# Kernel optimization log

Hardware: AMD Instinct MI355X
Metric: run time of the kernel (lower is better)

## Reference

```python
import jax, jax.numpy as jnp
import numpy as np

B, T, D, U = 64, 512, 256, 512


def setup_inputs() -> dict:
    key = jax.random.key(0)
    ks = jax.random.split(key, 7)
    s = 0.05  # keras 'uniform' init is small; small scale keeps gates unsaturated
    return {
        "x": jax.random.normal(ks[0], (B, T, D), dtype=jnp.float32),
        "w_xi": jax.random.normal(ks[1], (D, U), dtype=jnp.float32) * s,
        "w_xf": jax.random.normal(ks[2], (D, U), dtype=jnp.float32) * s,
        "w_xc": jax.random.normal(ks[3], (D, U), dtype=jnp.float32) * s,
        "w_hi": jax.random.normal(ks[4], (U, U), dtype=jnp.float32) * s,
        "w_hf": jax.random.normal(ks[5], (U, U), dtype=jnp.float32) * s,
        "w_hc": jax.random.normal(ks[6], (U, U), dtype=jnp.float32) * s,
        "b_i": jnp.zeros((1, U), dtype=jnp.float32),
        "b_f": jnp.zeros((1, U), dtype=jnp.float32),
        "b_c": jnp.zeros((1, U), dtype=jnp.float32),
        "h0": jnp.zeros((B, U), dtype=jnp.float32),
        "c0": jnp.zeros((B, U), dtype=jnp.float32),
    }


def reference(x, w_xi, w_xf, w_xc, w_hi, w_hf, w_hc, b_i, b_f, b_c, h0, c0):
    # Precompute input projections for all timesteps (batched GEMM), time-major.
    xi = (jnp.einsum('btd,du->btu', x, w_xi) + b_i).transpose(1, 0, 2)  # [T,B,U]
    xf = (jnp.einsum('btd,du->btu', x, w_xf) + b_f).transpose(1, 0, 2)
    xc = (jnp.einsum('btd,du->btu', x, w_xc) + b_c).transpose(1, 0, 2)

    def step(carry, xs):
        h, c = carry
        xi_t, xf_t, xc_t = xs
        i = jax.nn.sigmoid(xi_t + h @ w_hi)
        f = jax.nn.sigmoid(xf_t + h @ w_hf)
        c_in = jnp.tanh(xc_t + h @ w_hc)
        c_n = f * c + i * c_in
        h_n = jnp.tanh(c_n)  # output gate o == 1.0 in NOGLSTM
        return (h_n, c_n), h_n

    (_, _), hs = jax.lax.scan(step, (h0, c0), (xi, xf, xc))
    return hs.transpose(1, 0, 2)  # [B,T,U] full hidden sequence
```

## Files before the change

kernel.cpp:

```cpp
#include <hip/hip_runtime.h>
#include <stdint.h>

#define Bv 64
#define Tv 512
#define Dv 256
#define Uv 512
#define WPG 32

typedef __attribute__((ext_vector_type(8))) __bf16 bf16x8;
typedef __attribute__((ext_vector_type(8))) short short8;
typedef __attribute__((ext_vector_type(4))) float f32x4;

__device__ unsigned int g_flag[4 * WPG];
__device__ unsigned int g_gen[4 * WPG];
__device__ unsigned int g_hbuf[2 * Bv * Uv];

__device__ __forceinline__ unsigned int f2bf_bits(float x) {
    unsigned int u = __float_as_uint(x);
    return (u + 0x7fffu + ((u >> 16) & 1u)) >> 16;
}
__device__ __forceinline__ float bfbits2f(unsigned int b) {
    return __uint_as_float(b << 16);
}
__device__ __forceinline__ float fast_sigmoid(float x) {
    return __builtin_amdgcn_rcpf(1.f + __expf(-x));
}
__device__ __forceinline__ float fast_tanh(float x) {
    float ax = fabsf(x);
    float t  = __expf(-2.f * ax);
    float r  = (1.f - t) * __builtin_amdgcn_rcpf(1.f + t);
    return x < 0.f ? -r : r;
}

extern "C" __global__ void __launch_bounds__(256, 1)
noglstm_kernel(const float* __restrict__ x,
               const float* __restrict__ w_xi, const float* __restrict__ w_xf, const float* __restrict__ w_xc,
               const float* __restrict__ w_hi, const float* __restrict__ w_hf, const float* __restrict__ w_hc,
               const float* __restrict__ b_i, const float* __restrict__ b_f, const float* __restrict__ b_c,
               const float* __restrict__ h0, const float* __restrict__ c0,
               float* __restrict__ out)
{
    __shared__ f32x4 partLds[12 * 64];
    __shared__ float cTile[256];
    __shared__ float biasLds[48];
    __shared__ unsigned int baseLds;

    const int tid  = threadIdx.x;
    const int wg   = blockIdx.x;
    const int g    = wg >> 5;
    const int c    = wg & 31;
    const int r0   = g * 16;
    const int u0   = c * 16;
    const int wv   = tid >> 6;
    const int lane = tid & 63;
    const int n    = lane & 15;
    const int quad = lane >> 4;
    const int kh   = wv;
    const int m    = n;
    const int q    = quad;

    if (tid == 0) { unsigned v = g_gen[wg] + 1u; g_gen[wg] = v; baseLds = (v - 1u) * (unsigned)Tv; }
    if (tid < 16)      biasLds[tid]      = b_i[u0 + tid];
    else if (tid < 32) biasLds[tid]      = b_f[u0 + tid - 16];
    else if (tid < 48) biasLds[tid]      = b_c[u0 + tid - 32];
    cTile[tid] = c0[(size_t)(r0 + (tid >> 4)) * Uv + u0 + (tid & 15)];

    const float* WhP[3] = {w_hi, w_hf, w_hc};
    const float* WxP[3] = {w_xi, w_xf, w_xc};
    const int ucol = u0 + n;

    bf16x8 whHiR[3][4], whLoR[3][4], wxHiR[3][2], wxLoR[3][2];
    #pragma unroll
    for (int nt = 0; nt < 3; ++nt) {
        #pragma unroll
        for (int i = 0; i < 4; ++i) {
            short8 hi8, lo8;
            #pragma unroll
            for (int e = 0; e < 8; ++e) {
                int k = (kh * 4 + i) * 32 + quad * 8 + e;
                float w = WhP[nt][(size_t)k * Uv + ucol];
                unsigned int hb = f2bf_bits(w);
                unsigned int lb = f2bf_bits(w - bfbits2f(hb));
                hi8[e] = (short)hb; lo8[e] = (short)lb;
            }
            whHiR[nt][i] = __builtin_bit_cast(bf16x8, hi8);
            whLoR[nt][i] = __builtin_bit_cast(bf16x8, lo8);
        }
        #pragma unroll
        for (int i = 0; i < 2; ++i) {
            short8 hi8, lo8;
            #pragma unroll
            for (int e = 0; e < 8; ++e) {
                int k = (kh * 2 + i) * 32 + quad * 8 + e;
                float w = WxP[nt][(size_t)k * Uv + ucol];
                unsigned int hb = f2bf_bits(w);
                unsigned int lb = f2bf_bits(w - bfbits2f(hb));
                hi8[e] = (short)hb; lo8[e] = (short)lb;
            }
            wxHiR[nt][i] = __builtin_bit_cast(bf16x8, hi8);
            wxLoR[nt][i] = __builtin_bit_cast(bf16x8, lo8);
        }
    }

    bf16x8 xaH[2], xaL[2];
    #pragma unroll
    for (int i = 0; i < 2; ++i) {
        int kt = kh * 2 + i;
        const float* p = x + ((size_t)(r0 + m) * Tv + 0) * Dv + kt * 32 + q * 8;
        f32x4 a = *(const f32x4*)p;
        f32x4 b = *(const f32x4*)(p + 4);
        short8 hi8, lo8;
        #pragma unroll
        for (int e = 0; e < 8; ++e) {
            float v = (e < 4) ? a[e] : b[e - 4];
            unsigned int hb = f2bf_bits(v);
            unsigned int lb = f2bf_bits(v - bfbits2f(hb));
            hi8[e] = (short)hb; lo8[e] = (short)lb;
        }
        xaH[i] = __builtin_bit_cast(bf16x8, hi8);
        xaL[i] = __builtin_bit_cast(bf16x8, lo8);
    }
    __syncthreads();
    const unsigned int base = baseLds;

    const unsigned int* fpw = g_flag + g * WPG + kh * 8;

    for (int t = 0; t < Tv; ++t) {
        const bool packed = (t != 0);
        const bool pfch = (t + 1 < Tv);
        unsigned int hw32[32];
        f32x4 hf[8];
        f32x4 xf[4];

        if (packed) {
            const unsigned int E = base + (unsigned)t;
            unsigned int fv = 0xFFFFFFFFu;
            unsigned int spins = 0;
            for (;;) {
                if (lane < 8)
                    fv = __hip_atomic_load(fpw + lane, __ATOMIC_RELAXED,
                                           __HIP_MEMORY_SCOPE_AGENT);
                if (__all((lane >= 8) || (fv >= E))) break;
                if (++spins > (1u << 20)) break;
                if (spins > 16) __builtin_amdgcn_s_sleep(1);
            }
            __asm__ volatile("" ::: "memory");

            const unsigned int* hb = g_hbuf + (size_t)((t - 1) & 1) * (Bv * Uv);
            #pragma unroll
            for (int i = 0; i < 4; ++i) {
                int kt = kh * 4 + i;
                const unsigned int* p = hb + (size_t)(kt * 32 + q * 8) * Bv + r0 + m;
                #pragma unroll
                for (int e = 0; e < 8; ++e)
                    hw32[i * 8 + e] = __hip_atomic_load(p + e * Bv, __ATOMIC_RELAXED,
                                                        __HIP_MEMORY_SCOPE_AGENT);
            }
        } else {
            #pragma unroll
            for (int i = 0; i < 4; ++i) {
                int kt = kh * 4 + i;
                const float* p = h0 + (size_t)(r0 + m) * Uv + kt * 32 + q * 8;
                hf[i * 2]     = *(const f32x4*)p;
                hf[i * 2 + 1] = *(const f32x4*)(p + 4);
            }
        }

        if (pfch) {
            #pragma unroll
            for (int i = 0; i < 2; ++i) {
                int kt = kh * 2 + i;
                const float* p = x + ((size_t)(r0 + m) * Tv + (t + 1)) * Dv + kt * 32 + q * 8;
                xf[i * 2]     = *(const f32x4*)p;
                xf[i * 2 + 1] = *(const f32x4*)(p + 4);
            }
        }

        f32x4 acc[3], accX[3];
        #pragma unroll
        for (int nt = 0; nt < 3; ++nt) { acc[nt] = f32x4{0.f,0.f,0.f,0.f}; accX[nt] = f32x4{0.f,0.f,0.f,0.f}; }
        #pragma unroll
        for (int i = 0; i < 2; ++i) {
            #pragma unroll
            for (int nt = 0; nt < 3; ++nt) {
                accX[nt] = __builtin_amdgcn_mfma_f32_16x16x32_bf16(xaH[i], wxHiR[nt][i], accX[nt], 0, 0, 0);
                accX[nt] = __builtin_amdgcn_mfma_f32_16x16x32_bf16(xaH[i], wxLoR[nt][i], accX[nt], 0, 0, 0);
                accX[nt] = __builtin_amdgcn_mfma_f32_16x16x32_bf16(xaL[i], wxHiR[nt][i], accX[nt], 0, 0, 0);
                accX[nt] = __builtin_amdgcn_mfma_f32_16x16x32_bf16(xaL[i], wxLoR[nt][i], accX[nt], 0, 0, 0);
            }
        }

        #pragma unroll
        for (int i = 0; i < 4; ++i) {
            bf16x8 haH, haL;
            if (packed) {
                short8 hi8, lo8;
                #pragma unroll
                for (int e = 0; e < 8; ++e) {
                    unsigned int d = hw32[i * 8 + e];
                    hi8[e] = (short)(d >> 16);
                    lo8[e] = (short)(d & 0xffffu);
                }
                haH = __builtin_bit_cast(bf16x8, hi8);
                haL = __builtin_bit_cast(bf16x8, lo8);
            } else {
                short8 hi8, lo8;
                #pragma unroll
                for (int e = 0; e < 8; ++e) {
                    float v = (e < 4) ? hf[i * 2][e] : hf[i * 2 + 1][e - 4];
                    unsigned int hb2 = f2bf_bits(v);
                    unsigned int lb2 = f2bf_bits(v - bfbits2f(hb2));
                    hi8[e] = (short)hb2; lo8[e] = (short)lb2;
                }
                haH = __builtin_bit_cast(bf16x8, hi8);
                haL = __builtin_bit_cast(bf16x8, lo8);
            }
            #pragma unroll
            for (int nt = 0; nt < 3; ++nt) {
                acc[nt] = __builtin_amdgcn_mfma_f32_16x16x32_bf16(haH, whHiR[nt][i], acc[nt], 0, 0, 0);
                acc[nt] = __builtin_amdgcn_mfma_f32_16x16x32_bf16(haH, whLoR[nt][i], acc[nt], 0, 0, 0);
                acc[nt] = __builtin_amdgcn_mfma_f32_16x16x32_bf16(haL, whHiR[nt][i], acc[nt], 0, 0, 0);
                acc[nt] = __builtin_amdgcn_mfma_f32_16x16x32_bf16(haL, whLoR[nt][i], acc[nt], 0, 0, 0);
            }
        }

        #pragma unroll
        for (int nt = 0; nt < 3; ++nt) {
            acc[nt][0] += accX[nt][0]; acc[nt][1] += accX[nt][1];
            acc[nt][2] += accX[nt][2]; acc[nt][3] += accX[nt][3];
            partLds[(wv * 3 + nt) * 64 + lane] = acc[nt];
        }
        __syncthreads();

        const int r = tid >> 4, uu = tid & 15;
        float hn;
        {
            int plane = (r >> 2) * 16 + uu;
            int reg = r & 3;
            const float* pf2 = (const float*)partLds;
            float pi = biasLds[uu], pF = biasLds[16 + uu], pc = biasLds[32 + uu];
            #pragma unroll
            for (int w = 0; w < 4; ++w) {
                pi += pf2[((w * 3 + 0) * 64 + plane) * 4 + reg];
                pF += pf2[((w * 3 + 1) * 64 + plane) * 4 + reg];
                pc += pf2[((w * 3 + 2) * 64 + plane) * 4 + reg];
            }
            float iv  = fast_sigmoid(pi);
            float fv  = fast_sigmoid(pF);
            float cin = fast_tanh(pc);
            float cn  = fv * cTile[tid] + iv * cin;
            cTile[tid] = cn;
            hn = fast_tanh(cn);
            unsigned int hbb = f2bf_bits(hn);
            unsigned int lbb = f2bf_bits(hn - bfbits2f(hbb));
            __hip_atomic_store(g_hbuf + (size_t)(t & 1) * (Bv * Uv)
                               + (size_t)(u0 + uu) * Bv + (r0 + r),
                               (hbb << 16) | lbb, __ATOMIC_RELAXED,
                               __HIP_MEMORY_SCOPE_AGENT);
        }

        __asm__ volatile("s_waitcnt vmcnt(0)" ::: "memory");
        __syncthreads();
        if (tid == 0)
            __hip_atomic_store(&g_flag[g * WPG + c], base + (unsigned)t + 1u,
                               __ATOMIC_RELAXED, __HIP_MEMORY_SCOPE_AGENT);

        out[((size_t)(r0 + r) * Tv + t) * Uv + u0 + uu] = hn;

        if (pfch) {
            #pragma unroll
            for (int i = 0; i < 2; ++i) {
                short8 hi8, lo8;
                #pragma unroll
                for (int e = 0; e < 8; ++e) {
                    float v = (e < 4) ? xf[i * 2][e] : xf[i * 2 + 1][e - 4];
                    unsigned int hb2 = f2bf_bits(v);
                    unsigned int lb2 = f2bf_bits(v - bfbits2f(hb2));
                    hi8[e] = (short)hb2; lo8[e] = (short)lb2;
                }
                xaH[i] = __builtin_bit_cast(bf16x8, hi8);
                xaL[i] = __builtin_bit_cast(bf16x8, lo8);
            }
        }
        __syncthreads();
    }
}

extern "C" void kernel_launch(void* const* d_in, const int* in_sizes, int n_in,
                              void* d_out, int out_size, void* d_ws, size_t ws_size,
                              hipStream_t stream) {
    (void)in_sizes; (void)n_in; (void)out_size; (void)d_ws; (void)ws_size;
    noglstm_kernel<<<dim3(128), dim3(256), 0, stream>>>(
        (const float*)d_in[0],
        (const float*)d_in[1], (const float*)d_in[2], (const float*)d_in[3],
        (const float*)d_in[4], (const float*)d_in[5], (const float*)d_in[6],
        (const float*)d_in[7], (const float*)d_in[8], (const float*)d_in[9],
        (const float*)d_in[10], (const float*)d_in[11],
        (float*)d_out);
}
```

Measured before the change: 2.325 ms.

## Pack hidden-state exchange into 64-bit loads and move x prefetch off the critical path

Changes the global hidden-state buffer layout so adjacent unit pairs sit together, which lets each lane read h with 16 64-bit atomic loads in place of 32 32-bit loads. The next timestep's x is now issued as raw fp32 loads at the end of the step, and the bf16 hi/lo split is done at the start of the next step, overlapping the load latency with the flag spin. The trailing __syncthreads at the end of each timestep is removed, which saves one barrier per step but relies on the remaining barriers to protect shared-memory reuse across iterations.

```diff
diff --git a/kernel.cpp b/kernel.cpp
--- a/kernel.cpp
+++ b/kernel.cpp
@@ -10,10 +10,11 @@
 typedef __attribute__((ext_vector_type(8))) __bf16 bf16x8;
 typedef __attribute__((ext_vector_type(8))) short short8;
 typedef __attribute__((ext_vector_type(4))) float f32x4;
+typedef unsigned long long u64;
 
 __device__ unsigned int g_flag[4 * WPG];
 __device__ unsigned int g_gen[4 * WPG];
-__device__ unsigned int g_hbuf[2 * Bv * Uv];
+__device__ u64 g_hbuf[2 * Bv * Uv / 2];
 
 __device__ __forceinline__ unsigned int f2bf_bits(float x) {
     unsigned int u = __float_as_uint(x);
@@ -102,23 +103,13 @@
         }
     }
 
-    bf16x8 xaH[2], xaL[2];
+    f32x4 xf[4];
     #pragma unroll
     for (int i = 0; i < 2; ++i) {
         int kt = kh * 2 + i;
         const float* p = x + ((size_t)(r0 + m) * Tv + 0) * Dv + kt * 32 + q * 8;
-        f32x4 a = *(const f32x4*)p;
-        f32x4 b = *(const f32x4*)(p + 4);
-        short8 hi8, lo8;
-        #pragma unroll
-        for (int e = 0; e < 8; ++e) {
-            float v = (e < 4) ? a[e] : b[e - 4];
-            unsigned int hb = f2bf_bits(v);
-            unsigned int lb = f2bf_bits(v - bfbits2f(hb));
-            hi8[e] = (short)hb; lo8[e] = (short)lb;
-        }
-        xaH[i] = __builtin_bit_cast(bf16x8, hi8);
-        xaL[i] = __builtin_bit_cast(bf16x8, lo8);
+        xf[i * 2]     = *(const f32x4*)p;
+        xf[i * 2 + 1] = *(const f32x4*)(p + 4);
     }
     __syncthreads();
     const unsigned int base = baseLds;
@@ -128,9 +119,8 @@
     for (int t = 0; t < Tv; ++t) {
         const bool packed = (t != 0);
         const bool pfch = (t + 1 < Tv);
-        unsigned int hw32[32];
+        u64 hw64[16];
         f32x4 hf[8];
-        f32x4 xf[4];
 
         if (packed) {
             const unsigned int E = base + (unsigned)t;
@@ -146,14 +136,15 @@
             }
             __asm__ volatile("" ::: "memory");
 
-            const unsigned int* hb = g_hbuf + (size_t)((t - 1) & 1) * (Bv * Uv);
+            const u64* hb = g_hbuf + (size_t)((t - 1) & 1) * (Bv * Uv / 2);
             #pragma unroll
             for (int i = 0; i < 4; ++i) {
                 int kt = kh * 4 + i;
-                const unsigned int* p = hb + (size_t)(kt * 32 + q * 8) * Bv + r0 + m;
+                const u64* p = hb + (size_t)(kt * 16 + q * 4) * Bv + r0 + m;
                 #pragma unroll
-                for (int e = 0; e < 8; ++e)
-                    hw32[i * 8 + e] = __hip_atomic_load(p + e * Bv, __ATOMIC_RELAXED,
+                for (int j = 0; j < 4; ++j)
+                    hw64[i * 4 + j] = __hip_atomic_load(p + (size_t)j * Bv,
+                                                        __ATOMIC_RELAXED,
                                                         __HIP_MEMORY_SCOPE_AGENT);
             }
         } else {
@@ -166,14 +157,19 @@
             }
         }
 
-        if (pfch) {
-            #pragma unroll
-            for (int i = 0; i < 2; ++i) {
-                int kt = kh * 2 + i;
-                const float* p = x + ((size_t)(r0 + m) * Tv + (t + 1)) * Dv + kt * 32 + q * 8;
-                xf[i * 2]     = *(const f32x4*)p;
-                xf[i * 2 + 1] = *(const f32x4*)(p + 4);
-            }
+        bf16x8 xaH[2], xaL[2];
+        #pragma unroll
+        for (int i = 0; i < 2; ++i) {
+            short8 hi8, lo8;
+            #pragma unroll
+            for (int e = 0; e < 8; ++e) {
+                float v = (e < 4) ? xf[i * 2][e] : xf[i * 2 + 1][e - 4];
+                unsigned int hb2 = f2bf_bits(v);
+                unsigned int lb2 = f2bf_bits(v - bfbits2f(hb2));
+                hi8[e] = (short)hb2; lo8[e] = (short)lb2;
+            }
+            xaH[i] = __builtin_bit_cast(bf16x8, hi8);
+            xaL[i] = __builtin_bit_cast(bf16x8, lo8);
         }
 
         f32x4 acc[3], accX[3];
@@ -196,10 +192,14 @@
             if (packed) {
                 short8 hi8, lo8;
                 #pragma unroll
-                for (int e = 0; e < 8; ++e) {
-                    unsigned int d = hw32[i * 8 + e];
-                    hi8[e] = (short)(d >> 16);
-                    lo8[e] = (short)(d & 0xffffu);
+                for (int j = 0; j < 4; ++j) {
+                    u64 w = hw64[i * 4 + j];
+                    unsigned int d0 = (unsigned int)w;
+                    unsigned int d1 = (unsigned int)(w >> 32);
+                    hi8[2 * j]     = (short)(d0 >> 16);
+                    lo8[2 * j]     = (short)(d0 & 0xffffu);
+                    hi8[2 * j + 1] = (short)(d1 >> 16);
+                    lo8[2 * j + 1] = (short)(d1 & 0xffffu);
                 }
                 haH = __builtin_bit_cast(bf16x8, hi8);
                 haL = __builtin_bit_cast(bf16x8, lo8);
@@ -253,9 +253,10 @@
             hn = fast_tanh(cn);
             unsigned int hbb = f2bf_bits(hn);
             unsigned int lbb = f2bf_bits(hn - bfbits2f(hbb));
-            __hip_atomic_store(g_hbuf + (size_t)(t & 1) * (Bv * Uv)
-                               + (size_t)(u0 + uu) * Bv + (r0 + r),
-                               (hbb << 16) | lbb, __ATOMIC_RELAXED,
+            unsigned int* hb32 = (unsigned int*)g_hbuf;
+            size_t di = (size_t)(t & 1) * (Bv * Uv)
+                      + ((size_t)((u0 + uu) >> 1) * Bv + (r0 + r)) * 2 + (uu & 1);
+            __hip_atomic_store(hb32 + di, (hbb << 16) | lbb, __ATOMIC_RELAXED,
                                __HIP_MEMORY_SCOPE_AGENT);
         }
 
@@ -270,19 +271,12 @@
         if (pfch) {
             #pragma unroll
             for (int i = 0; i < 2; ++i) {
-                short8 hi8, lo8;
-                #pragma unroll
-                for (int e = 0; e < 8; ++e) {
-                    float v = (e < 4) ? xf[i * 2][e] : xf[i * 2 + 1][e - 4];
-                    unsigned int hb2 = f2bf_bits(v);
-                    unsigned int lb2 = f2bf_bits(v - bfbits2f(hb2));
-                    hi8[e] = (short)hb2; lo8[e] = (short)lb2;
-                }
-                xaH[i] = __builtin_bit_cast(bf16x8, hi8);
-                xaL[i] = __builtin_bit_cast(bf16x8, lo8);
-            }
-        }
-        __syncthreads();
+                int kt = kh * 2 + i;
+                const float* p = x + ((size_t)(r0 + m) * Tv + (t + 1)) * Dv + kt * 32 + q * 8;
+                xf[i * 2]     = *(const f32x4*)p;
+                xf[i * 2 + 1] = *(const f32x4*)(p + 4);
+            }
+        }
     }
 }
 
```

Result: no change. 2.304 ms (-0.9%).
